# Performance work log

Hardware: AMD Instinct MI355X
Metric: run time of the kernel (lower is better)

## Reference

```python
import jax, jax.numpy as jnp
import numpy as np

B, N, D = 32, 2048, 512
K = 64          # cluster_size
G = 16          # ghost_clusters
BN_EPS = 1e-5
L2_EPS = 1e-12


def setup_inputs() -> dict:
    key = jax.random.key(0)
    k1, k2, k3 = jax.random.split(key, 3)
    init_sc = 1.0 / np.sqrt(D)
    x = jax.random.normal(k1, (B, N, D), dtype=jnp.float32)
    clusters = init_sc * jax.random.normal(k2, (D, K + G), dtype=jnp.float32)
    clusters2 = init_sc * jax.random.normal(k3, (D, K), dtype=jnp.float32)
    bn_gamma = jnp.ones((K + G,), dtype=jnp.float32)
    bn_beta = jnp.zeros((K + G,), dtype=jnp.float32)
    return {"x": x, "clusters": clusters, "clusters2": clusters2,
            "bn_gamma": bn_gamma, "bn_beta": bn_beta}


def _l2norm(v, axis):
    n = jnp.sqrt(jnp.sum(v * v, axis=axis, keepdims=True))
    return v / jnp.maximum(n, L2_EPS)


def reference(x, clusters, clusters2, bn_gamma, bn_beta):
    b, n, d = x.shape
    kc = clusters2.shape[1]
    # projection: [B*N, K+G]
    a = x.reshape(-1, d) @ clusters
    # BatchNorm1d (training mode: batch statistics, biased variance)
    mean = jnp.mean(a, axis=0)
    var = jnp.mean((a - mean) ** 2, axis=0)
    a = (a - mean) * jax.lax.rsqrt(var + BN_EPS) * bn_gamma + bn_beta
    # softmax over all clusters, drop ghost clusters
    a = jax.nn.softmax(a, axis=1)[:, :kc].reshape(b, n, kc)
    # fused VLAD: v[b,d,k] = sum_n a[b,n,k] * (x[b,n,d] - c2[d,k])
    a_sum = jnp.sum(a, axis=1)                              # [B, K]
    vlad = jnp.einsum('bnd,bnk->bdk', x, a)                 # [B, D, K]
    vlad = vlad - clusters2[None, :, :] * a_sum[:, None, :]
    # intra-normalize over D, flatten, global L2 normalize
    vlad = _l2norm(vlad, axis=1)
    vlad = vlad.reshape(b, kc * d)
    vlad = _l2norm(vlad, axis=1)
    return vlad
```

## Files before the change

### kernel.cpp

```cpp
#include <hip/hip_runtime.h>
#include <hip/hip_bf16.h>

#define B_ 32
#define N_ 2048
#define D_ 512
#define KC_ 64
#define KG_ 80
#define M_ (B_*N_)

typedef __attribute__((ext_vector_type(8))) short short8;
typedef __attribute__((ext_vector_type(4))) float f32x4;

__device__ __forceinline__ unsigned short bf_rn(float f){
  unsigned int u = __float_as_uint(f);
  unsigned int r = u + 0x7FFFu + ((u >> 16) & 1u);
  return (unsigned short)(r >> 16);
}
__device__ __forceinline__ float bf_up(unsigned short h){
  return __uint_as_float(((unsigned int)h) << 16);
}
__device__ __forceinline__ void cvt8(const float* v, short8& hi, short8& lo){
#pragma unroll
  for (int i=0;i<8;i++){
    unsigned short h = bf_rn(v[i]);
    float rem = v[i] - bf_up(h);
    hi[i] = (short)h;
    lo[i] = (short)bf_rn(rem);
  }
}

__global__ __launch_bounds__(256) void k0_prep(const float* __restrict__ cl,
                                               unsigned short* __restrict__ Bf)
{
  int tid = blockIdx.x*256 + threadIdx.x;
  int l  = tid & 63;
  int hl = (tid >> 6) & 1;
  int j  = (tid >> 7) % 5;
  int c  = tid / 640;
  int kk  = c*32 + (l>>4)*8;
  int col = j*16 + (l&15);
  unsigned short o[8];
#pragma unroll
  for (int jj=0;jj<8;jj++){
    float v = cl[(size_t)(kk+jj)*KG_ + col];
    unsigned short h = bf_rn(v);
    if (hl == 0) o[jj] = h;
    else         o[jj] = bf_rn(v - bf_up(h));
  }
#pragma unroll
  for (int jj=0;jj<8;jj++) Bf[(size_t)tid*8 + jj] = o[jj];
}

__global__ __launch_bounds__(256) void k1_proj(
    const float* __restrict__ x, const unsigned short* __restrict__ Bf,
    float* __restrict__ a, float* __restrict__ S1, float* __restrict__ S2)
{
  __shared__ float ls1[KG_], ls2[KG_];
  const int t = threadIdx.x;
  const int w = t >> 6, lane = t & 63;
  const int m = lane & 15, q = lane >> 4;
  const int row0 = blockIdx.x*128 + w*32;
  if (t < KG_){ ls1[t]=0.f; ls2[t]=0.f; }

  const float* xr0 = x + (size_t)(row0 + m)*D_ + q*8;
  const float* xr1 = xr0 + (size_t)16*D_;

  f32x4 acc[2][5];
#pragma unroll
  for (int rt=0;rt<2;rt++)
#pragma unroll
    for (int j=0;j<5;j++) acc[rt][j] = (f32x4){0.f,0.f,0.f,0.f};

  for (int c=0;c<16;c++){
    float v0[8], v1[8];
    *(float4*)&v0[0] = *(const float4*)(xr0 + c*32);
    *(float4*)&v0[4] = *(const float4*)(xr0 + c*32 + 4);
    *(float4*)&v1[0] = *(const float4*)(xr1 + c*32);
    *(float4*)&v1[4] = *(const float4*)(xr1 + c*32 + 4);
    short8 ah0, al0, ah1, al1;
    cvt8(v0, ah0, al0);
    cvt8(v1, ah1, al1);
    const unsigned short* bp = Bf + (size_t)(c*5)*1024 + lane*8;
#pragma unroll
    for (int j=0;j<5;j++){
      short8 bhi = *(const short8*)(bp + (size_t)j*1024);
      short8 blo = *(const short8*)(bp + (size_t)j*1024 + 512);
      acc[0][j] = __builtin_amdgcn_mfma_f32_16x16x32_bf16(ah0, bhi, acc[0][j], 0,0,0);
      acc[0][j] = __builtin_amdgcn_mfma_f32_16x16x32_bf16(al0, bhi, acc[0][j], 0,0,0);
      acc[0][j] = __builtin_amdgcn_mfma_f32_16x16x32_bf16(ah0, blo, acc[0][j], 0,0,0);
      acc[1][j] = __builtin_amdgcn_mfma_f32_16x16x32_bf16(ah1, bhi, acc[1][j], 0,0,0);
      acc[1][j] = __builtin_amdgcn_mfma_f32_16x16x32_bf16(al1, bhi, acc[1][j], 0,0,0);
      acc[1][j] = __builtin_amdgcn_mfma_f32_16x16x32_bf16(ah1, blo, acc[1][j], 0,0,0);
    }
  }

  float s1v[5] = {0,0,0,0,0}, s2v[5] = {0,0,0,0,0};
#pragma unroll
  for (int rt=0;rt<2;rt++){
#pragma unroll
    for (int j=0;j<5;j++){
      f32x4 v = acc[rt][j];
      size_t base = (size_t)(row0 + rt*16 + q*4)*KG_ + j*16 + m;
      a[base]        = v[0];
      a[base+KG_]    = v[1];
      a[base+2*KG_]  = v[2];
      a[base+3*KG_]  = v[3];
      s1v[j] += v[0]+v[1]+v[2]+v[3];
      s2v[j] += v[0]*v[0]+v[1]*v[1]+v[2]*v[2]+v[3]*v[3];
    }
  }
#pragma unroll
  for (int j=0;j<5;j++){
    float s1 = s1v[j], s2 = s2v[j];
    s1 += __shfl_xor(s1,16); s1 += __shfl_xor(s1,32);
    s2 += __shfl_xor(s2,16); s2 += __shfl_xor(s2,32);
    if (q == 0){
      atomicAdd(&ls1[j*16+m], s1);
      atomicAdd(&ls2[j*16+m], s2);
    }
  }
  __syncthreads();
  if (t < KG_){ atomicAdd(&S1[t], ls1[t]); atomicAdd(&S2[t], ls2[t]); }
}

__global__ void k2_bn(const float* __restrict__ S1, const float* __restrict__ S2,
                      const float* __restrict__ gamma, const float* __restrict__ beta,
                      float* __restrict__ scale, float* __restrict__ shift)
{
  int t = threadIdx.x;
  if (t < KG_){
    const float invM = 1.0f / (float)M_;
    float mean = S1[t] * invM;
    float var  = S2[t] * invM - mean*mean;
    float sc = gamma[t] * rsqrtf(var + 1e-5f);
    scale[t] = sc;
    shift[t] = beta[t] - mean*sc;
  }
}

__global__ __launch_bounds__(256) void k3_softmax(
    float* __restrict__ a, const float* __restrict__ scale,
    const float* __restrict__ shift, float* __restrict__ asum)
{
  __shared__ float as[64*84];
  __shared__ float sc[KG_], sh[KG_];
  __shared__ float lsum[KC_];
  unsigned int* p32 = (unsigned int*)a;
  const int t = threadIdx.x;
  const int row0 = blockIdx.x * 64;
  if (t < KG_){ sc[t]=scale[t]; sh[t]=shift[t]; }
  if (t < KC_) lsum[t]=0.f;
  __syncthreads();
#pragma unroll
  for (int l=0;l<20;l++){
    int idx = t + 256*l;
    int r = idx/80, col = idx - r*80;
    float v = a[(size_t)(row0+r)*KG_ + col];
    as[r*84+col] = v*sc[col] + sh[col];
  }
  __syncthreads();
  const int rt = t >> 2;
  const int g  = t & 3;
  float m = -1e30f;
#pragma unroll
  for (int c=0;c<20;c++) m = fmaxf(m, as[rt*84 + g + 4*c]);
  m = fmaxf(m, __shfl_xor(m,1));
  m = fmaxf(m, __shfl_xor(m,2));
  float e[20]; float s = 0.f;
#pragma unroll
  for (int c=0;c<20;c++){ float v = __expf(as[rt*84 + g + 4*c] - m); e[c]=v; s+=v; }
  s += __shfl_xor(s,1);
  s += __shfl_xor(s,2);
  const float inv = 1.f/s;
#pragma unroll
  for (int c=0;c<16;c++){
    int col = g + 4*c;
    float pv = e[c]*inv;
    unsigned short h = bf_rn(pv);
    unsigned short lo = bf_rn(pv - bf_up(h));
    p32[(size_t)(row0+rt)*KG_ + col] = (unsigned int)h | ((unsigned int)lo << 16);
    float su = pv;
    su += __shfl_xor(su,4);  su += __shfl_xor(su,8);
    su += __shfl_xor(su,16); su += __shfl_xor(su,32);
    if ((t&63) < 4) atomicAdd(&lsum[col], su);
  }
  __syncthreads();
  if (t < KC_) atomicAdd(&asum[(blockIdx.x>>5)*KC_ + t], lsum[t]);
}

__global__ __launch_bounds__(256,4) void k4_vlad(
    const float* __restrict__ x, const unsigned int* __restrict__ p32,
    float* __restrict__ vp)
{
  __shared__ unsigned short xh[2][2048], xl[2][2048];
  __shared__ unsigned short ph[2][2048], pl[2][2048];
  const int t = threadIdx.x;
  const int blk = blockIdx.x;
  const int ns = blk & 3;
  const int dt = (blk >> 2) & 7;
  const int b  = blk >> 5;
  const int w = t >> 6, lane = t & 63;
  const int m = lane & 15, q = lane >> 4;
  const int d0 = dt*64;
  const int nbase = ns*512;

  const float*        xbase = x   + ((size_t)b*N_ + nbase + q*8)*D_  + d0 + w*16 + m;
  const unsigned int* pbase = p32 + ((size_t)b*N_ + nbase + q*8)*KG_ + w*16 + m;

  f32x4 acc[4];
#pragma unroll
  for (int j=0;j<4;j++) acc[j] = (f32x4){0.f,0.f,0.f,0.f};

  float v[8]; unsigned int u[8];
#pragma unroll
  for (int jj=0;jj<8;jj++) v[jj] = xbase[(size_t)jj*D_];
#pragma unroll
  for (int jj=0;jj<8;jj++) u[jj] = pbase[(size_t)jj*KG_];
  {
    short8 hi, lo; cvt8(v, hi, lo);
    *(short8*)&xh[0][t*8] = hi;
    *(short8*)&xl[0][t*8] = lo;
    short8 hp, lp;
#pragma unroll
    for (int jj=0;jj<8;jj++){ hp[jj] = (short)(u[jj] & 0xFFFFu); lp[jj] = (short)(u[jj] >> 16); }
    *(short8*)&ph[0][t*8] = hp;
    *(short8*)&pl[0][t*8] = lp;
  }

  int cur = 0;
  for (int c=0;c<16;c++){
    __syncthreads();
    if (c < 15){
      const float*        xp = xbase + (size_t)(c+1)*32*D_;
      const unsigned int* pp = pbase + (size_t)(c+1)*32*KG_;
#pragma unroll
      for (int jj=0;jj<8;jj++) v[jj] = xp[(size_t)jj*D_];
#pragma unroll
      for (int jj=0;jj<8;jj++) u[jj] = pp[(size_t)jj*KG_];
    }
    short8 ahi = *(const short8*)&xh[cur][(w*64+lane)*8];
    short8 alo = *(const short8*)&xl[cur][(w*64+lane)*8];
#pragma unroll
    for (int j=0;j<4;j++){
      short8 bhi = *(const short8*)&ph[cur][(j*64+lane)*8];
      short8 blo = *(const short8*)&pl[cur][(j*64+lane)*8];
      acc[j] = __builtin_amdgcn_mfma_f32_16x16x32_bf16(ahi, bhi, acc[j], 0,0,0);
      acc[j] = __builtin_amdgcn_mfma_f32_16x16x32_bf16(alo, bhi, acc[j], 0,0,0);
      acc[j] = __builtin_amdgcn_mfma_f32_16x16x32_bf16(ahi, blo, acc[j], 0,0,0);
    }
    if (c < 15){
      short8 hi, lo; cvt8(v, hi, lo);
      *(short8*)&xh[cur^1][t*8] = hi;
      *(short8*)&xl[cur^1][t*8] = lo;
      short8 hp, lp;
#pragma unroll
      for (int jj=0;jj<8;jj++){ hp[jj] = (short)(u[jj] & 0xFFFFu); lp[jj] = (short)(u[jj] >> 16); }
      *(short8*)&ph[cur^1][t*8] = hp;
      *(short8*)&pl[cur^1][t*8] = lp;
    }
    cur ^= 1;
  }
#pragma unroll
  for (int j=0;j<4;j++){
    f32x4 vv = acc[j];
    size_t base = (((size_t)ns*B_ + b)*D_ + d0 + w*16 + q*4)*KC_ + j*16 + m;
    vp[base]         = vv[0];
    vp[base +   KC_] = vv[1];
    vp[base + 2*KC_] = vv[2];
    vp[base + 3*KC_] = vv[3];
  }
}

__global__ __launch_bounds__(1024) void k5_norm(
    const float* __restrict__ vp, const float* __restrict__ c2,
    const float* __restrict__ asum, float* __restrict__ out)
{
  __shared__ float part[16][64];
  __shared__ float invd[64];
  __shared__ float gi_s;
  const int b = blockIdx.x;
  const int t = threadIdx.x;
  const int k = t & 63, dg = t >> 6;
  const float av = asum[b*KC_ + k];
  const size_t stride = (size_t)B_*D_*KC_;
  float v[32];
  float ss = 0.f;
#pragma unroll
  for (int s=0;s<32;s++){
    int d = dg + 16*s;
    size_t idx = ((size_t)b*D_ + d)*KC_ + k;
    float vv = 0.f;
#pragma unroll
    for (int nsp=0;nsp<4;nsp++) vv += vp[idx + (size_t)nsp*stride];
    vv -= c2[d*KC_ + k]*av;
    v[s] = vv;
    ss += vv*vv;
  }
  part[dg][k] = ss;
  __syncthreads();
  if (t < 64){
    float n2 = 0.f;
#pragma unroll
    for (int i=0;i<16;i++) n2 += part[i][t];
    float nn = sqrtf(n2);
    float denom = fmaxf(nn, 1e-12f);
    invd[t] = 1.f/denom;
    float ratio = nn/denom;
    float r2 = ratio*ratio;
#pragma unroll
    for (int mm=1;mm<64;mm<<=1) r2 += __shfl_xor(r2, mm);
    if (t==0){
      float g = sqrtf(r2);
      gi_s = 1.f/fmaxf(g, 1e-12f);
    }
  }
  __syncthreads();
  const float gi = gi_s;
  const float ik = invd[k];
#pragma unroll
  for (int s=0;s<32;s++){
    int d = dg + 16*s;
    out[(size_t)b*(D_*KC_) + (size_t)d*KC_ + k] = v[s]*ik*gi;
  }
}

extern "C" void kernel_launch(void* const* d_in, const int* in_sizes, int n_in,
                              void* d_out, int out_size, void* d_ws, size_t ws_size,
                              hipStream_t stream)
{
  const float* x     = (const float*)d_in[0];
  const float* cl    = (const float*)d_in[1];
  const float* c2    = (const float*)d_in[2];
  const float* gamma = (const float*)d_in[3];
  const float* beta  = (const float*)d_in[4];
  float* out = (float*)d_out;
  float* ws  = (float*)d_ws;

  float* S1    = ws;
  float* S2    = ws + 80;
  float* scale = ws + 160;
  float* shift = ws + 240;
  float* asum  = ws + 320;
  unsigned short* Bf = (unsigned short*)(ws + 4096);
  float* a     = ws + 45056;
  float* vp    = a + (size_t)M_*KG_;

  hipMemsetAsync(ws, 0, 2368*sizeof(float), stream);
  k0_prep   <<<40,   256, 0, stream>>>(cl, Bf);
  k1_proj   <<<512,  256, 0, stream>>>(x, Bf, a, S1, S2);
  k2_bn     <<<1,    128, 0, stream>>>(S1, S2, gamma, beta, scale, shift);
  k3_softmax<<<1024, 256, 0, stream>>>(a, scale, shift, asum);
  k4_vlad   <<<1024, 256, 0, stream>>>(x, (const unsigned int*)a, vp);
  k5_norm   <<<32,  1024, 0, stream>>>(vp, c2, asum, out);
}
```

Before: 275.5 us.

## Fold BN finalize into softmax and split final normalization across more blocks

Removes the single-block BN statistics kernel by having every softmax block compute scale and shift from the accumulated sums itself. The final normalization kernel, previously 32 blocks of 1024 threads holding the data in registers, becomes two kernels of 256 blocks each. The first sums the partials, writes the intermediate VLAD to a reused workspace buffer and atomically accumulates per-cluster squared norms. The second applies the intra and global normalization. This adds a launch and an extra round trip of the VLAD tensor through memory in exchange for far more parallelism in the tail stage.

Result: faster. 266.6 us (-3.2%).

```diff
diff --git a/kernel.cpp b/kernel.cpp
--- a/kernel.cpp
+++ b/kernel.cpp
@@ -123,32 +123,25 @@
   if (t < KG_){ atomicAdd(&S1[t], ls1[t]); atomicAdd(&S2[t], ls2[t]); }
 }
 
-__global__ void k2_bn(const float* __restrict__ S1, const float* __restrict__ S2,
-                      const float* __restrict__ gamma, const float* __restrict__ beta,
-                      float* __restrict__ scale, float* __restrict__ shift)
-{
-  int t = threadIdx.x;
+__global__ __launch_bounds__(256) void k3_softmax(
+    float* __restrict__ a, const float* __restrict__ S1, const float* __restrict__ S2,
+    const float* __restrict__ gamma, const float* __restrict__ beta,
+    float* __restrict__ asum)
+{
+  __shared__ float as[64*84];
+  __shared__ float sc[KG_], sh[KG_];
+  __shared__ float lsum[KC_];
+  unsigned int* p32 = (unsigned int*)a;
+  const int t = threadIdx.x;
+  const int row0 = blockIdx.x * 64;
   if (t < KG_){
     const float invM = 1.0f / (float)M_;
     float mean = S1[t] * invM;
     float var  = S2[t] * invM - mean*mean;
-    float sc = gamma[t] * rsqrtf(var + 1e-5f);
-    scale[t] = sc;
-    shift[t] = beta[t] - mean*sc;
-  }
-}
-
-__global__ __launch_bounds__(256) void k3_softmax(
-    float* __restrict__ a, const float* __restrict__ scale,
-    const float* __restrict__ shift, float* __restrict__ asum)
-{
-  __shared__ float as[64*84];
-  __shared__ float sc[KG_], sh[KG_];
-  __shared__ float lsum[KC_];
-  unsigned int* p32 = (unsigned int*)a;
-  const int t = threadIdx.x;
-  const int row0 = blockIdx.x * 64;
-  if (t < KG_){ sc[t]=scale[t]; sh[t]=shift[t]; }
+    float scv = gamma[t] * rsqrtf(var + 1e-5f);
+    sc[t] = scv;
+    sh[t] = beta[t] - mean*scv;
+  }
   if (t < KC_) lsum[t]=0.f;
   __syncthreads();
 #pragma unroll
@@ -271,37 +264,48 @@
   }
 }
 
-__global__ __launch_bounds__(1024) void k5_norm(
+__global__ __launch_bounds__(256) void k5a(
     const float* __restrict__ vp, const float* __restrict__ c2,
-    const float* __restrict__ asum, float* __restrict__ out)
-{
-  __shared__ float part[16][64];
-  __shared__ float invd[64];
-  __shared__ float gi_s;
-  const int b = blockIdx.x;
+    const float* __restrict__ asum, float* __restrict__ vbuf,
+    float* __restrict__ ssq)
+{
+  __shared__ float red[4][64];
+  const int blk = blockIdx.x;
+  const int b = blk >> 3, ds = blk & 7;
   const int t = threadIdx.x;
   const int k = t & 63, dg = t >> 6;
   const float av = asum[b*KC_ + k];
   const size_t stride = (size_t)B_*D_*KC_;
-  float v[32];
   float ss = 0.f;
 #pragma unroll
-  for (int s=0;s<32;s++){
-    int d = dg + 16*s;
+  for (int s=0;s<16;s++){
+    int d = ds*64 + dg + 4*s;
     size_t idx = ((size_t)b*D_ + d)*KC_ + k;
-    float vv = 0.f;
-#pragma unroll
-    for (int nsp=0;nsp<4;nsp++) vv += vp[idx + (size_t)nsp*stride];
+    float vv = vp[idx] + vp[idx+stride] + vp[idx+2*stride] + vp[idx+3*stride];
     vv -= c2[d*KC_ + k]*av;
-    v[s] = vv;
+    vbuf[idx] = vv;
     ss += vv*vv;
   }
-  part[dg][k] = ss;
+  red[dg][k] = ss;
   __syncthreads();
   if (t < 64){
-    float n2 = 0.f;
-#pragma unroll
-    for (int i=0;i<16;i++) n2 += part[i][t];
+    float v = red[0][t] + red[1][t] + red[2][t] + red[3][t];
+    atomicAdd(&ssq[b*KC_ + t], v);
+  }
+}
+
+__global__ __launch_bounds__(256) void k5b(
+    const float* __restrict__ vbuf, const float* __restrict__ ssq,
+    float* __restrict__ out)
+{
+  __shared__ float invd[64];
+  __shared__ float gi_s;
+  const int blk = blockIdx.x;
+  const int b = blk >> 3, ds = blk & 7;
+  const int t = threadIdx.x;
+  const int k = t & 63, dg = t >> 6;
+  if (t < 64){
+    float n2 = ssq[b*KC_ + t];
     float nn = sqrtf(n2);
     float denom = fmaxf(nn, 1e-12f);
     invd[t] = 1.f/denom;
@@ -310,17 +314,16 @@
 #pragma unroll
     for (int mm=1;mm<64;mm<<=1) r2 += __shfl_xor(r2, mm);
     if (t==0){
-      float g = sqrtf(r2);
-      gi_s = 1.f/fmaxf(g, 1e-12f);
-    }
-  }
-  __syncthreads();
-  const float gi = gi_s;
-  const float ik = invd[k];
-#pragma unroll
-  for (int s=0;s<32;s++){
-    int d = dg + 16*s;
-    out[(size_t)b*(D_*KC_) + (size_t)d*KC_ + k] = v[s]*ik*gi;
+      gi_s = 1.f/fmaxf(sqrtf(r2), 1e-12f);
+    }
+  }
+  __syncthreads();
+  const float gik = gi_s * invd[k];
+#pragma unroll
+  for (int s=0;s<16;s++){
+    int d = ds*64 + dg + 4*s;
+    size_t idx = ((size_t)b*D_ + d)*KC_ + k;
+    out[idx] = vbuf[idx]*gik;
   }
 }
 
@@ -338,18 +341,17 @@
 
   float* S1    = ws;
   float* S2    = ws + 80;
-  float* scale = ws + 160;
-  float* shift = ws + 240;
-  float* asum  = ws + 320;
-  unsigned short* Bf = (unsigned short*)(ws + 4096);
-  float* a     = ws + 45056;
+  float* asum  = ws + 160;
+  float* ssq   = ws + 2208;
+  unsigned short* Bf = (unsigned short*)(ws + 4608);
+  float* a     = ws + 45568;
   float* vp    = a + (size_t)M_*KG_;
 
-  hipMemsetAsync(ws, 0, 2368*sizeof(float), stream);
+  hipMemsetAsync(ws, 0, 4608*sizeof(float), stream);
   k0_prep   <<<40,   256, 0, stream>>>(cl, Bf);
   k1_proj   <<<512,  256, 0, stream>>>(x, Bf, a, S1, S2);
-  k2_bn     <<<1,    128, 0, stream>>>(S1, S2, gamma, beta, scale, shift);
-  k3_softmax<<<1024, 256, 0, stream>>>(a, scale, shift, asum);
+  k3_softmax<<<1024, 256, 0, stream>>>(a, S1, S2, gamma, beta, asum);
   k4_vlad   <<<1024, 256, 0, stream>>>(x, (const unsigned int*)a, vp);
-  k5_norm   <<<32,  1024, 0, stream>>>(vp, c2, asum, out);
-}
+  k5a       <<<256,  256, 0, stream>>>(vp, c2, asum, a, ssq);
+  k5b       <<<256,  256, 0, stream>>>(a, ssq, out);
+}
```
